# Optimization experiments

Measured on AMD Instinct MI355X. Metric: run time of the kernel, lower is better.

## Reference

```python
import jax, jax.numpy as jnp
import numpy as np

G, K, H = 4, 8, 512  # gate_dim, k blocks, block size

def setup_inputs() -> dict:
    key = jax.random.key(0)
    kx, kA, kB = jax.random.split(key, 3)
    x = jax.random.normal(kx, (4096, K * H), dtype=jnp.float32)
    # xavier_normal for (h,h) matrices: std = sqrt(2/(h+h)) = 1/sqrt(h)
    std = 1.0 / np.sqrt(H)
    A = jax.random.normal(kA, (G, H, H), dtype=jnp.float32) * std
    B = jax.random.normal(kB, (G, H, H), dtype=jnp.float32) * std
    return {"x": x, "A": A, "B": B}

def reference(x, A, B):
    # W = blockdiag-style: row block (g,i), col block j -> A_g if i==j else B_g.
    # y[b, g, i, :] = x_i @ A_g^T + (sum_j x_j - x_i) @ B_g^T
    #              = x_i @ (A_g - B_g)^T + S @ B_g^T
    bsz = x.shape[0]
    x3 = x.reshape(bsz, K, H)                      # [B, k, h]
    S = x3.sum(axis=1)                              # [B, h]
    diag_part = jnp.einsum('bkh,gph->bgkp', x3, A - B)   # [B, g, k, h]
    sum_part = jnp.einsum('bh,gph->bgp', S, B)           # [B, g, h]
    out = diag_part + sum_part[:, :, None, :]
    return out.reshape(bsz, G * K * H)
```

## Files before the change

kernel.cpp:

```cpp
#include <hip/hip_runtime.h>

typedef _Float16 f16x8 __attribute__((ext_vector_type(8)));
typedef _Float16 f16x4 __attribute__((ext_vector_type(4)));
typedef _Float16 f16x2 __attribute__((ext_vector_type(2)));
typedef float f32x4 __attribute__((ext_vector_type(4)));
typedef float f32x2 __attribute__((ext_vector_type(2)));

#define GLD_LDS16(gp, lp)                                                        \
  __builtin_amdgcn_global_load_lds(                                              \
      (const __attribute__((address_space(1))) void*)(gp),                       \
      (__attribute__((address_space(3))) void*)(lp), 16, 0, 0)

__global__ void prep_weights_k(const float* __restrict__ A, const float* __restrict__ B,
                               _Float16* __restrict__ Cw, _Float16* __restrict__ Bw) {
  int gid = blockIdx.x * 256 + threadIdx.x;
  f32x4 a = ((const f32x4*)A)[gid];
  f32x4 b = ((const f32x4*)B)[gid];
  f16x4 c, bb;
  c.x = (_Float16)(a.x - b.x); c.y = (_Float16)(a.y - b.y);
  c.z = (_Float16)(a.z - b.z); c.w = (_Float16)(a.w - b.w);
  bb.x = (_Float16)b.x; bb.y = (_Float16)b.y;
  bb.z = (_Float16)b.z; bb.w = (_Float16)b.w;
  ((f16x4*)Cw)[gid] = c;
  ((f16x4*)Bw)[gid] = bb;
}

__global__ void prep_x_k(const float* __restrict__ x, _Float16* __restrict__ xh,
                         _Float16* __restrict__ Sh) {
  int b = blockIdx.x, t = threadIdx.x;
  const f32x2* xr = (const f32x2*)(x + (size_t)b * 4096);
  f16x2* xo = (f16x2*)xh + (size_t)b * 2048;
  float s0 = 0.f, s1 = 0.f;
#pragma unroll
  for (int i = 0; i < 8; ++i) {
    f32x2 v = xr[i * 256 + t];
    f16x2 h;
    h.x = (_Float16)v.x; h.y = (_Float16)v.y;
    xo[i * 256 + t] = h;
    s0 += v.x; s1 += v.y;
  }
  f16x2 sv;
  sv.x = (_Float16)s0; sv.y = (_Float16)s1;
  ((f16x2*)Sh)[(size_t)b * 256 + t] = sv;
}

template <int MODE>
__global__ __launch_bounds__(256) void gemm_k(const _Float16* __restrict__ Am,
                                              const _Float16* __restrict__ W,
                                              const float* __restrict__ tvec,
                                              float* __restrict__ out) {
  __shared__ __align__(16) _Float16 lA[128 * 32];
  __shared__ __align__(16) _Float16 lB[128 * 32];

  const int tid = threadIdx.x;
  const int lane = tid & 63;
  const int wv = tid >> 6;
  const int tile_n = blockIdx.x & 15;
  const int tile_m = blockIdx.x >> 4;

  const _Float16* gA[2];
  const _Float16* gB[2];
  _Float16* lpA[2];
  _Float16* lpB[2];
#pragma unroll
  for (int i = 0; i < 2; ++i) {
    int c = i * 256 + tid;
    int row = c >> 2;
    int lc = (c & 3) ^ ((row >> 1) & 3);
    gA[i] = Am + ((size_t)(tile_m * 128 + row) * 512 + lc * 8);
    gB[i] = W + ((size_t)(tile_n * 128 + row) * 512 + lc * 8);
    lpA[i] = &lA[(size_t)(i * 256 + wv * 64) * 8];
    lpB[i] = &lB[(size_t)(i * 256 + wv * 64) * 8];
  }

  const int lm = lane & 15;
  const int q = lane >> 4;
  const int mw = (wv >> 1) * 64;
  const int nw = (wv & 1) * 64;

  int aoff[4], boff[4];
#pragma unroll
  for (int f = 0; f < 4; ++f) {
    int rA = mw + f * 16 + lm;
    aoff[f] = rA * 32 + (q ^ ((rA >> 1) & 3)) * 8;
    int rB = nw + f * 16 + lm;
    boff[f] = rB * 32 + (q ^ ((rB >> 1) & 3)) * 8;
  }

  f32x4 acc[4][4];
#pragma unroll
  for (int im = 0; im < 4; ++im)
#pragma unroll
    for (int in = 0; in < 4; ++in) acc[im][in] = (f32x4){0.f, 0.f, 0.f, 0.f};

  for (int kt = 0; kt < 16; ++kt) {
    __syncthreads();
#pragma unroll
    for (int i = 0; i < 2; ++i) {
      GLD_LDS16(gA[i] + kt * 32, lpA[i]);
      GLD_LDS16(gB[i] + kt * 32, lpB[i]);
    }
    __syncthreads();
    f16x8 af[4], bf[4];
#pragma unroll
    for (int f = 0; f < 4; ++f) {
      af[f] = *(const f16x8*)&lA[aoff[f]];
      bf[f] = *(const f16x8*)&lB[boff[f]];
    }
#pragma unroll
    for (int im = 0; im < 4; ++im)
#pragma unroll
      for (int in = 0; in < 4; ++in)
        acc[im][in] =
            __builtin_amdgcn_mfma_f32_16x16x32_f16(af[im], bf[in], acc[im][in], 0, 0, 0);
  }

#pragma unroll
  for (int im = 0; im < 4; ++im) {
    const int mbase = tile_m * 128 + mw + im * 16 + q * 4;
#pragma unroll
    for (int in = 0; in < 4; ++in) {
      const int col = tile_n * 128 + nw + in * 16 + lm;
      f32x4 v = acc[im][in];
      if (MODE == 1) {
        const int b = mbase >> 3;
        const float tv = tvec[(size_t)b * 2048 + col];
        float* op = out + (size_t)b * 16384 + (size_t)(col >> 9) * 4096 +
                    (size_t)(mbase & 7) * 512 + (col & 511);
#pragma unroll
        for (int r = 0; r < 4; ++r) op[r * 512] = v[r] + tv;
      } else {
        float* op = out + (size_t)mbase * 2048 + col;
#pragma unroll
        for (int r = 0; r < 4; ++r) op[(size_t)r * 2048] = v[r];
      }
    }
  }
}

extern "C" void kernel_launch(void* const* d_in, const int* in_sizes, int n_in,
                              void* d_out, int out_size, void* d_ws, size_t ws_size,
                              hipStream_t stream) {
  const float* x = (const float*)d_in[0];
  const float* A = (const float*)d_in[1];
  const float* B = (const float*)d_in[2];
  float* out = (float*)d_out;
  char* ws = (char*)d_ws;

  _Float16* xh = (_Float16*)(ws);
  _Float16* Sh = (_Float16*)(ws + 33554432u);
  _Float16* Cw = (_Float16*)(ws + 37748736u);
  _Float16* Bw = (_Float16*)(ws + 39845888u);
  float* tv = (float*)(ws + 41943040u);

  prep_weights_k<<<1024, 256, 0, stream>>>(A, B, Cw, Bw);
  prep_x_k<<<4096, 256, 0, stream>>>(x, xh, Sh);
  gemm_k<0><<<512, 256, 0, stream>>>(Sh, Bw, nullptr, tv);
  gemm_k<1><<<4096, 256, 0, stream>>>(xh, Cw, tv, out);
}
```

Measured before the change: 419.4 us.

## Merge prep kernels, widen main GEMM N-tile, store bias in fp16, nontemporal output

Merges the x and weight conversion kernels into one launch. The main GEMM is templated on N-tile width and runs with 256-wide N tiles (NT=2), which halves the block count and reuses each A tile across twice the columns. The S@B bias is now stored as fp16 instead of fp32, reducing its traffic. Output stores use nontemporal hints. The wider tile doubles accumulator registers per thread, which may cut occupancy, and the fp16 bias adds rounding error.

```diff
diff --git a/kernel.cpp b/kernel.cpp
--- a/kernel.cpp
+++ b/kernel.cpp
@@ -11,106 +11,106 @@
       (const __attribute__((address_space(1))) void*)(gp),                       \
       (__attribute__((address_space(3))) void*)(lp), 16, 0, 0)
 
-__global__ void prep_weights_k(const float* __restrict__ A, const float* __restrict__ B,
-                               _Float16* __restrict__ Cw, _Float16* __restrict__ Bw) {
-  int gid = blockIdx.x * 256 + threadIdx.x;
-  f32x4 a = ((const f32x4*)A)[gid];
-  f32x4 b = ((const f32x4*)B)[gid];
-  f16x4 c, bb;
-  c.x = (_Float16)(a.x - b.x); c.y = (_Float16)(a.y - b.y);
-  c.z = (_Float16)(a.z - b.z); c.w = (_Float16)(a.w - b.w);
-  bb.x = (_Float16)b.x; bb.y = (_Float16)b.y;
-  bb.z = (_Float16)b.z; bb.w = (_Float16)b.w;
-  ((f16x4*)Cw)[gid] = c;
-  ((f16x4*)Bw)[gid] = bb;
+__global__ void prep_k(const float* __restrict__ x, const float* __restrict__ A,
+                       const float* __restrict__ B, _Float16* __restrict__ xh,
+                       _Float16* __restrict__ Sh, _Float16* __restrict__ Cw,
+                       _Float16* __restrict__ Bw) {
+  const int t = threadIdx.x;
+  if (blockIdx.x < 4096) {
+    const int b = blockIdx.x;
+    const f32x2* xr = (const f32x2*)(x + (size_t)b * 4096);
+    f16x2* xo = (f16x2*)xh + (size_t)b * 2048;
+    float s0 = 0.f, s1 = 0.f;
+#pragma unroll
+    for (int i = 0; i < 8; ++i) {
+      f32x2 v = xr[i * 256 + t];
+      f16x2 h;
+      h.x = (_Float16)v.x; h.y = (_Float16)v.y;
+      xo[i * 256 + t] = h;
+      s0 += v.x; s1 += v.y;
+    }
+    f16x2 sv;
+    sv.x = (_Float16)s0; sv.y = (_Float16)s1;
+    ((f16x2*)Sh)[(size_t)b * 256 + t] = sv;
+  } else {
+    const int gid = (blockIdx.x - 4096) * 256 + t;
+    f32x4 a = ((const f32x4*)A)[gid];
+    f32x4 b4 = ((const f32x4*)B)[gid];
+    f16x4 c, bb;
+    c.x = (_Float16)(a.x - b4.x); c.y = (_Float16)(a.y - b4.y);
+    c.z = (_Float16)(a.z - b4.z); c.w = (_Float16)(a.w - b4.w);
+    bb.x = (_Float16)b4.x; bb.y = (_Float16)b4.y;
+    bb.z = (_Float16)b4.z; bb.w = (_Float16)b4.w;
+    ((f16x4*)Cw)[gid] = c;
+    ((f16x4*)Bw)[gid] = bb;
+  }
 }
 
-__global__ void prep_x_k(const float* __restrict__ x, _Float16* __restrict__ xh,
-                         _Float16* __restrict__ Sh) {
-  int b = blockIdx.x, t = threadIdx.x;
-  const f32x2* xr = (const f32x2*)(x + (size_t)b * 4096);
-  f16x2* xo = (f16x2*)xh + (size_t)b * 2048;
-  float s0 = 0.f, s1 = 0.f;
-#pragma unroll
-  for (int i = 0; i < 8; ++i) {
-    f32x2 v = xr[i * 256 + t];
-    f16x2 h;
-    h.x = (_Float16)v.x; h.y = (_Float16)v.y;
-    xo[i * 256 + t] = h;
-    s0 += v.x; s1 += v.y;
-  }
-  f16x2 sv;
-  sv.x = (_Float16)s0; sv.y = (_Float16)s1;
-  ((f16x2*)Sh)[(size_t)b * 256 + t] = sv;
-}
-
-template <int MODE>
+template <int MODE, int NT>
 __global__ __launch_bounds__(256) void gemm_k(const _Float16* __restrict__ Am,
                                               const _Float16* __restrict__ W,
-                                              const float* __restrict__ tvec,
-                                              float* __restrict__ out) {
+                                              const _Float16* __restrict__ tvec,
+                                              float* __restrict__ outf,
+                                              _Float16* __restrict__ outh) {
+  constexpr int BN = 128 * NT;
+  constexpr int NTN = 2048 / BN;
   __shared__ __align__(16) _Float16 lA[128 * 32];
-  __shared__ __align__(16) _Float16 lB[128 * 32];
+  __shared__ __align__(16) _Float16 lB[BN * 32];
 
   const int tid = threadIdx.x;
   const int lane = tid & 63;
   const int wv = tid >> 6;
-  const int tile_n = blockIdx.x & 15;
-  const int tile_m = blockIdx.x >> 4;
+  const int tile_n = blockIdx.x % NTN;
+  const int tile_m = blockIdx.x / NTN;
 
-  const _Float16* gA[2];
-  const _Float16* gB[2];
-  _Float16* lpA[2];
-  _Float16* lpB[2];
-#pragma unroll
-  for (int i = 0; i < 2; ++i) {
-    int c = i * 256 + tid;
-    int row = c >> 2;
-    int lc = (c & 3) ^ ((row >> 1) & 3);
-    gA[i] = Am + ((size_t)(tile_m * 128 + row) * 512 + lc * 8);
-    gB[i] = W + ((size_t)(tile_n * 128 + row) * 512 + lc * 8);
-    lpA[i] = &lA[(size_t)(i * 256 + wv * 64) * 8];
-    lpB[i] = &lB[(size_t)(i * 256 + wv * 64) * 8];
-  }
+  const int row0 = tid >> 2;
+  const int lc0 = (tid & 3) ^ ((row0 >> 1) & 3);
+  const _Float16* gA0 = Am + ((size_t)(tile_m * 128 + row0) * 512 + lc0 * 8);
+  const _Float16* gB0 = W + ((size_t)(tile_n * BN + row0) * 512 + lc0 * 8);
+  _Float16* lpA0 = &lA[(size_t)(wv * 64) * 8];
+  _Float16* lpB0 = &lB[(size_t)(wv * 64) * 8];
 
   const int lm = lane & 15;
   const int q = lane >> 4;
   const int mw = (wv >> 1) * 64;
-  const int nw = (wv & 1) * 64;
+  const int nw = (wv & 1) * (64 * NT);
 
-  int aoff[4], boff[4];
+  int aoff[4], boff[4 * NT];
 #pragma unroll
   for (int f = 0; f < 4; ++f) {
     int rA = mw + f * 16 + lm;
     aoff[f] = rA * 32 + (q ^ ((rA >> 1) & 3)) * 8;
+  }
+#pragma unroll
+  for (int f = 0; f < 4 * NT; ++f) {
     int rB = nw + f * 16 + lm;
     boff[f] = rB * 32 + (q ^ ((rB >> 1) & 3)) * 8;
   }
 
-  f32x4 acc[4][4];
+  f32x4 acc[4][4 * NT];
 #pragma unroll
   for (int im = 0; im < 4; ++im)
 #pragma unroll
-    for (int in = 0; in < 4; ++in) acc[im][in] = (f32x4){0.f, 0.f, 0.f, 0.f};
+    for (int in = 0; in < 4 * NT; ++in) acc[im][in] = (f32x4){0.f, 0.f, 0.f, 0.f};
 
   for (int kt = 0; kt < 16; ++kt) {
     __syncthreads();
 #pragma unroll
-    for (int i = 0; i < 2; ++i) {
-      GLD_LDS16(gA[i] + kt * 32, lpA[i]);
-      GLD_LDS16(gB[i] + kt * 32, lpB[i]);
-    }
+    for (int i = 0; i < 2; ++i)
+      GLD_LDS16(gA0 + (size_t)i * (64 * 512) + kt * 32, lpA0 + i * 256 * 8);
+#pragma unroll
+    for (int i = 0; i < 2 * NT; ++i)
+      GLD_LDS16(gB0 + (size_t)i * (64 * 512) + kt * 32, lpB0 + i * 256 * 8);
     __syncthreads();
-    f16x8 af[4], bf[4];
+    f16x8 af[4], bf[4 * NT];
 #pragma unroll
-    for (int f = 0; f < 4; ++f) {
-      af[f] = *(const f16x8*)&lA[aoff[f]];
-      bf[f] = *(const f16x8*)&lB[boff[f]];
-    }
+    for (int f = 0; f < 4; ++f) af[f] = *(const f16x8*)&lA[aoff[f]];
+#pragma unroll
+    for (int f = 0; f < 4 * NT; ++f) bf[f] = *(const f16x8*)&lB[boff[f]];
 #pragma unroll
     for (int im = 0; im < 4; ++im)
 #pragma unroll
-      for (int in = 0; in < 4; ++in)
+      for (int in = 0; in < 4 * NT; ++in)
         acc[im][in] =
             __builtin_amdgcn_mfma_f32_16x16x32_f16(af[im], bf[in], acc[im][in], 0, 0, 0);
   }
@@ -118,21 +118,28 @@
 #pragma unroll
   for (int im = 0; im < 4; ++im) {
     const int mbase = tile_m * 128 + mw + im * 16 + q * 4;
+    if (MODE == 1) {
+      const int b = mbase >> 3;
+      float* ob = outf + (size_t)b * 16384 + (size_t)(mbase & 7) * 512;
+      const _Float16* tb = tvec + (size_t)b * 2048;
 #pragma unroll
-    for (int in = 0; in < 4; ++in) {
-      const int col = tile_n * 128 + nw + in * 16 + lm;
-      f32x4 v = acc[im][in];
-      if (MODE == 1) {
-        const int b = mbase >> 3;
-        const float tv = tvec[(size_t)b * 2048 + col];
-        float* op = out + (size_t)b * 16384 + (size_t)(col >> 9) * 4096 +
-                    (size_t)(mbase & 7) * 512 + (col & 511);
+      for (int in = 0; in < 4 * NT; ++in) {
+        const int col = tile_n * BN + nw + in * 16 + lm;
+        const float tv = (float)tb[col];
+        float* op = ob + (size_t)(col >> 9) * 4096 + (col & 511);
+        f32x4 v = acc[im][in];
 #pragma unroll
-        for (int r = 0; r < 4; ++r) op[r * 512] = v[r] + tv;
-      } else {
-        float* op = out + (size_t)mbase * 2048 + col;
+        for (int r = 0; r < 4; ++r)
+          __builtin_nontemporal_store(v[r] + tv, op + r * 512);
+      }
+    } else {
+      _Float16* ob = outh + (size_t)mbase * 2048;
 #pragma unroll
-        for (int r = 0; r < 4; ++r) op[(size_t)r * 2048] = v[r];
+      for (int in = 0; in < 4 * NT; ++in) {
+        const int col = tile_n * BN + nw + in * 16 + lm;
+        f32x4 v = acc[im][in];
+#pragma unroll
+        for (int r = 0; r < 4; ++r) ob[(size_t)r * 2048 + col] = (_Float16)v[r];
       }
     }
   }
@@ -151,10 +158,9 @@
   _Float16* Sh = (_Float16*)(ws + 33554432u);
   _Float16* Cw = (_Float16*)(ws + 37748736u);
   _Float16* Bw = (_Float16*)(ws + 39845888u);
-  float* tv = (float*)(ws + 41943040u);
+  _Float16* tvh = (_Float16*)(ws + 41943040u);
 
-  prep_weights_k<<<1024, 256, 0, stream>>>(A, B, Cw, Bw);
-  prep_x_k<<<4096, 256, 0, stream>>>(x, xh, Sh);
-  gemm_k<0><<<512, 256, 0, stream>>>(Sh, Bw, nullptr, tv);
-  gemm_k<1><<<4096, 256, 0, stream>>>(xh, Cw, tv, out);
+  prep_k<<<5120, 256, 0, stream>>>(x, A, B, xh, Sh, Cw, Bw);
+  gemm_k<0, 1><<<512, 256, 0, stream>>>(Sh, Bw, nullptr, nullptr, tvh);
+  gemm_k<1, 2><<<2048, 256, 0, stream>>>(xh, Cw, tvh, out, nullptr);
 }
```

After: 472.6 us. 12.7% more time.
